# Optimization experiments

Hardware: AMD Instinct MI355X
Metric: run time of the kernel (lower is better)

## Reference

```python
import jax, jax.numpy as jnp
import numpy as np

EPS = 1e-07


def _softsplat(tenIn, tenFlow):
    # tenIn: [N, C, H, W], tenFlow: [N, 2, H, W]
    N, C, H, W = tenIn.shape
    dtype = tenIn.dtype
    gridX = jnp.arange(W, dtype=dtype)[None, None, :]  # [1,1,W]
    gridY = jnp.arange(H, dtype=dtype)[None, :, None]  # [1,H,1]
    fltX = gridX + tenFlow[:, 0]  # [N,H,W]
    fltY = gridY + tenFlow[:, 1]  # [N,H,W]
    finite = jnp.isfinite(fltX) & jnp.isfinite(fltY)
    fltX = jnp.where(finite, fltX, 0.0)
    fltY = jnp.where(finite, fltY, 0.0)
    nwX = jnp.floor(fltX)
    nwY = jnp.floor(fltY)
    b = jnp.arange(N, dtype=jnp.int32)[:, None, None]  # [N,1,1]
    tenIn_flat = jnp.transpose(tenIn, (0, 2, 3, 1)).reshape(-1, C)  # [N*H*W, C]
    out = jnp.zeros((N * H * W, C), dtype=dtype)
    # four bilinear corners: NW, NE, SW, SE
    for dx, dy in ((0, 0), (1, 0), (0, 1), (1, 1)):
        ix = nwX + dx
        iy = nwY + dy
        # bilinear weight, e.g. NW: (nwX+1-fltX)*(nwY+1-fltY)
        w = (1.0 - jnp.abs(fltX - ix)) * (1.0 - jnp.abs(fltY - iy))
        valid = finite & (ix >= 0) & (ix < W) & (iy >= 0) & (iy < H)
        w = jnp.where(valid, w, 0.0)  # zero-weight replaces torch's masked select
        ixi = jnp.clip(ix.astype(jnp.int32), 0, W - 1)
        iyi = jnp.clip(iy.astype(jnp.int32), 0, H - 1)
        idx = (b * (H * W) + iyi * W + ixi).reshape(-1)  # [N*H*W]
        out = out.at[idx].add(tenIn_flat * w.reshape(-1, 1))
    return jnp.transpose(out.reshape(N, H, W, C), (0, 3, 1, 2))


def setup_inputs() -> dict:
    key = jax.random.key(0)
    k1, k2, k3 = jax.random.split(key, 3)
    N, C, H, W = 4, 3, 1080, 1920
    tenIn = jax.random.normal(k1, (N, C, H, W), dtype=jnp.float32)
    tenFlow = jax.random.normal(k2, (N, 2, H, W), dtype=jnp.float32)
    tenMetric = jax.random.normal(k3, (N, 1, H, W), dtype=jnp.float32)
    return {"tenIn": tenIn, "tenFlow": tenFlow, "tenMetric": tenMetric}


def reference(tenIn, tenFlow, tenMetric):
    # mode='soft': concat [tenIn * exp(metric), exp(metric)], splat, normalize
    m = jnp.exp(tenMetric)
    tenCat = jnp.concatenate([tenIn * m, m], axis=1)  # [N, C+1, H, W]
    tenOut = _softsplat(tenCat, tenFlow)
    # mode_sub is None -> addeps normalization
    return tenOut[:, :-1] / (tenOut[:, -1:] + EPS)
```

## Files before the change

kernel.cpp:

```cpp
#include <hip/hip_runtime.h>
#include <math.h>

#define EPS 1e-7f

constexpr int Nn = 4, Hh = 1080, Ww = 1920;
constexpr int HW = Hh * Ww;
constexpr int TOTAL = Nn * HW;

constexpr int TW = 32, TH = 32;
constexpr int TXN = 60, TYN = 34;
constexpr int REACH = 5;
constexpr float NEAR_MAX = 5.0f;
constexpr int WINW = TW + 2 * REACH;
constexpr int WINH = TH + 2 * REACH;
constexpr int WINSZ = WINW * WINH;
constexpr int NCW = TW + 1;
constexpr int NCH = TH + 1;
constexpr int NCELLS = NCW * NCH;
constexpr int CNT_PAD = 1280;
constexpr int PADL = 8;
constexpr int NCHUNK = 12;
constexpr int TOTCH = NCHUNK * WINH;


__global__ __launch_bounds__(256) void far_scatter(
    const float* __restrict__ tenIn, const float* __restrict__ tenFlow,
    const float* __restrict__ tenMetric,
    unsigned int* __restrict__ farCount, float* __restrict__ farList,
    unsigned int farCap)
{
    int q = blockIdx.x * 256 + threadIdx.x;
    if (q >= TOTAL / 4) return;
    int n  = q / (HW / 4);
    int p  = (q - n * (HW / 4)) * 4;

    const float* __restrict__ f0 = tenFlow + (size_t)(n * 2 + 0) * HW;
    const float* __restrict__ f1 = f0 + HW;
    float4 fx4 = *(const float4*)(f0 + p);
    float4 fy4 = *(const float4*)(f1 + p);

    float mx = fmaxf(fmaxf(fabsf(fx4.x), fabsf(fx4.y)), fmaxf(fabsf(fx4.z), fabsf(fx4.w)));
    float my = fmaxf(fmaxf(fabsf(fy4.x), fabsf(fy4.y)), fmaxf(fabsf(fy4.z), fabsf(fy4.w)));
    if (!(mx > NEAR_MAX || my > NEAR_MAX)) return;

    int y = p / Ww;
    int xbase = p - y * Ww;
    float fxa[4] = {fx4.x, fx4.y, fx4.z, fx4.w};
    float fya[4] = {fy4.x, fy4.y, fy4.z, fy4.w};

#pragma unroll
    for (int k = 0; k < 4; ++k) {
        float fxv = fxa[k], fyv = fya[k];
        if (!(fabsf(fxv) > NEAR_MAX || fabsf(fyv) > NEAR_MAX)) continue;
        float fx = (float)(xbase + k) + fxv;
        float fy = (float)y + fyv;
        if (!isfinite(fx) || !isfinite(fy)) continue;
        if (!(fx > -1.0f && fx < (float)Ww && fy > -1.0f && fy < (float)Hh)) continue;

        int pp = p + k;
        float m  = expf(tenMetric[(size_t)n * HW + pp]);
        float v0 = tenIn[((size_t)n * 3 + 0) * HW + pp] * m;
        float v1 = tenIn[((size_t)n * 3 + 1) * HW + pp] * m;
        float v2 = tenIn[((size_t)n * 3 + 2) * HW + pp] * m;

        unsigned int slot = atomicAdd(farCount, 1u);
        if (slot < farCap) {
            float* ep = farList + (size_t)slot * 8;
            ep[0] = __int_as_float(n);
            ep[1] = fx; ep[2] = fy;
            ep[3] = v0; ep[4] = v1; ep[5] = v2; ep[6] = m;
            ep[7] = 0.0f;
        }
    }
}


__global__ __launch_bounds__(256, 3) void gather_splat(
    const float* __restrict__ tenIn, const float* __restrict__ tenFlow,
    const float* __restrict__ tenMetric,
    const float* __restrict__ farList, const unsigned int* __restrict__ farCount,
    unsigned int farCap, float* __restrict__ out)
{
    __shared__ float2 sFrac[WINSZ];
    __shared__ float4 sVal[WINSZ];
    __shared__ unsigned int sOff[CNT_PAD];
    __shared__ unsigned int sWsum[8];

    const int tx = blockIdx.x, ty = blockIdx.y, n = blockIdx.z;
    const int tX = tx * TW, tY = ty * TH;
    const int tid = threadIdx.x;

    for (int j = tid; j < CNT_PAD; j += 256) sOff[j] = 0u;
    __syncthreads();

    const float* __restrict__ f0 = tenFlow   + (size_t)(n * 2 + 0) * HW;
    const float* __restrict__ f1 = tenFlow   + (size_t)(n * 2 + 1) * HW;
    const float* __restrict__ mp = tenMetric + (size_t)n * HW;
    const float* __restrict__ i0 = tenIn + (size_t)(n * 3 + 0) * HW;
    const float* __restrict__ i1 = tenIn + (size_t)(n * 3 + 1) * HW;
    const float* __restrict__ i2 = tenIn + (size_t)(n * 3 + 2) * HW;

    unsigned int pk[2][4];
    float sfx[2][4], swy[2][4];

#pragma unroll
    for (int cc = 0; cc < 2; ++cc) {
#pragma unroll
        for (int k = 0; k < 4; ++k) { pk[cc][k] = 0xFFFFFFFFu; sfx[cc][k] = 0.f; swy[cc][k] = 0.f; }
        int cidx = tid + cc * 256;
        if (cidx >= TOTCH) continue;
        int wy = cidx / NCHUNK;
        int cx = cidx - wy * NCHUNK;
        int sy = tY - REACH + wy;
        int gx = tX - PADL + cx * 4;
        if (sy < 0 || sy >= Hh || gx < 0 || gx > Ww - 4) continue;
        int p = sy * Ww + gx;
        float4 fx4 = *(const float4*)(f0 + p);
        float4 fy4 = *(const float4*)(f1 + p);
        float fxa[4] = {fx4.x, fx4.y, fx4.z, fx4.w};
        float fya[4] = {fy4.x, fy4.y, fy4.z, fy4.w};
#pragma unroll
        for (int k = 0; k < 4; ++k) {
            int x = gx + k;
            if (x < tX - REACH || x >= tX + TW + REACH) continue;
            float fxv = fxa[k], fyv = fya[k];
            if (!(fabsf(fxv) <= NEAR_MAX && fabsf(fyv) <= NEAR_MAX)) continue;
            float fx = (float)x + fxv;
            float fy = (float)sy + fyv;
            float flx = floorf(fx), fly = floorf(fy);
            int lx0 = (int)flx - tX;
            int ly0 = (int)fly - tY;
            if (lx0 < -1 || lx0 >= TW || ly0 < -1 || ly0 >= TH) continue;
            int ci = (ly0 + 1) * NCW + (lx0 + 1);
            unsigned int sic = atomicAdd(&sOff[ci], 1u);
            pk[cc][k] = (sic << 16) | (unsigned int)ci;
            sfx[cc][k] = fx;
            swy[cc][k] = fy - fly;
        }
    }
    __syncthreads();

    unsigned int c0v, c1v, c2v, c3v, c4v;
    {
        int base = tid * 5;
        c0v = sOff[base];     c1v = sOff[base + 1]; c2v = sOff[base + 2];
        c3v = sOff[base + 3]; c4v = sOff[base + 4];
    }
    unsigned int tsum = c0v + c1v + c2v + c3v + c4v;
    unsigned int incl = tsum;
#pragma unroll
    for (int d = 1; d < 64; d <<= 1) {
        unsigned int v = __shfl_up(incl, d);
        if ((tid & 63) >= d) incl += v;
    }
    const int wv = tid >> 6;
    if ((tid & 63) == 63) sWsum[wv] = incl;
    __syncthreads();
    unsigned int woff = 0;
    {
        unsigned int w0 = sWsum[0], w1 = sWsum[1], w2 = sWsum[2];
        if (wv > 0) woff += w0;
        if (wv > 1) woff += w1;
        if (wv > 2) woff += w2;
    }
    unsigned int texcl = woff + incl - tsum;
    {
        int base = tid * 5;
        unsigned int o0 = texcl, o1 = o0 + c0v, o2 = o1 + c1v, o3 = o2 + c2v, o4 = o3 + c3v;
        sOff[base] = o0; sOff[base + 1] = o1; sOff[base + 2] = o2;
        sOff[base + 3] = o3; sOff[base + 4] = o4;
    }
    __syncthreads();

#pragma unroll
    for (int cc = 0; cc < 2; ++cc) {
        int cidx = tid + cc * 256;
        if (cidx >= TOTCH) continue;
        unsigned int allv = pk[cc][0] & pk[cc][1] & pk[cc][2] & pk[cc][3];
        if (allv == 0xFFFFFFFFu) continue;
        int wy = cidx / NCHUNK;
        int cx = cidx - wy * NCHUNK;
        int sy = tY - REACH + wy;
        int gx = tX - PADL + cx * 4;
        int p = sy * Ww + gx;
        float4 m4  = *(const float4*)(mp + p);
        float4 a04 = *(const float4*)(i0 + p);
        float4 a14 = *(const float4*)(i1 + p);
        float4 a24 = *(const float4*)(i2 + p);
        float ma[4]  = {m4.x,  m4.y,  m4.z,  m4.w};
        float a0a[4] = {a04.x, a04.y, a04.z, a04.w};
        float a1a[4] = {a14.x, a14.y, a14.z, a14.w};
        float a2a[4] = {a24.x, a24.y, a24.z, a24.w};
#pragma unroll
        for (int k = 0; k < 4; ++k) {
            unsigned int p_ = pk[cc][k];
            if (p_ == 0xFFFFFFFFu) continue;
            unsigned int ci  = p_ & 0xFFFFu;
            unsigned int sic = p_ >> 16;
            unsigned int slot = sOff[ci] + sic;
            float m = expf(ma[k]);
            sFrac[slot] = make_float2(sfx[cc][k], swy[cc][k]);
            sVal[slot]  = make_float4(a0a[k] * m, a1a[k] * m, a2a[k] * m, m);
        }
    }
    __syncthreads();

    const int r   = tid >> 3;
    const int g   = tid & 7;
    const int cc0 = g * 4;
    const float cx0f = (float)(tX + cc0);

    float4 acc0 = make_float4(0.f, 0.f, 0.f, 0.f);
    float4 acc1 = make_float4(0.f, 0.f, 0.f, 0.f);
    float4 acc2 = make_float4(0.f, 0.f, 0.f, 0.f);
    float4 acc3 = make_float4(0.f, 0.f, 0.f, 0.f);

    const unsigned int a0 = sOff[r * NCW + cc0];
    const unsigned int a1 = sOff[r * NCW + cc0 + 5];
    const unsigned int b0 = sOff[(r + 1) * NCW + cc0];
    const unsigned int b1 = sOff[(r + 1) * NCW + cc0 + 5];

#define SPLAT_BODY(AY_EXPR)                                               \
    do {                                                                  \
        float2 fr = sFrac[s];                                             \
        float4 v  = sVal[s];                                              \
        float ay  = (AY_EXPR);                                            \
        float dxf = fr.x - cx0f;                                          \
        float ax0 = fmaxf(0.f, 1.f - fabsf(dxf));                         \
        float ax1 = fmaxf(0.f, 1.f - fabsf(dxf - 1.f));                   \
        float ax2 = fmaxf(0.f, 1.f - fabsf(dxf - 2.f));                   \
        float ax3 = fmaxf(0.f, 1.f - fabsf(dxf - 3.f));                   \
        float w0 = ay * ax0, w1 = ay * ax1, w2 = ay * ax2, w3 = ay * ax3; \
        acc0.x += v.x * w0; acc0.y += v.y * w0; acc0.z += v.z * w0; acc0.w += v.w * w0; \
        acc1.x += v.x * w1; acc1.y += v.y * w1; acc1.z += v.z * w1; acc1.w += v.w * w1; \
        acc2.x += v.x * w2; acc2.y += v.y * w2; acc2.z += v.z * w2; acc2.w += v.w * w2; \
        acc3.x += v.x * w3; acc3.y += v.y * w3; acc3.z += v.z * w3; acc3.w += v.w * w3; \
    } while (0)

    for (unsigned int s = a0; s < a1; ++s) SPLAT_BODY(fr.y);
    for (unsigned int s = b0; s < b1; ++s) SPLAT_BODY(1.f - fr.y);
#undef SPLAT_BODY

    const int gy = tY + r;
    if (gy >= Hh) return;
    const int gx = tX + cc0;

    unsigned int fc = *farCount;
    if (fc > farCap) fc = farCap;
    const float gyf = (float)gy;
    const float gxf = (float)gx;
    for (unsigned int e = 0; e < fc; ++e) {
        const float* ep = farList + (size_t)e * 8;
        if (__float_as_int(ep[0]) != n) continue;
        float ffx = ep[1], ffy = ep[2];
        float ay = fmaxf(0.f, 1.f - fabsf(ffy - gyf));
        if (ay > 0.f) {
            float fv0 = ep[3], fv1 = ep[4], fv2 = ep[5], fm = ep[6];
            float d = ffx - gxf;
            float ax0 = fmaxf(0.f, 1.f - fabsf(d));
            float ax1 = fmaxf(0.f, 1.f - fabsf(d - 1.f));
            float ax2 = fmaxf(0.f, 1.f - fabsf(d - 2.f));
            float ax3 = fmaxf(0.f, 1.f - fabsf(d - 3.f));
            float w0 = ay * ax0, w1 = ay * ax1, w2 = ay * ax2, w3 = ay * ax3;
            acc0.x += fv0 * w0; acc0.y += fv1 * w0; acc0.z += fv2 * w0; acc0.w += fm * w0;
            acc1.x += fv0 * w1; acc1.y += fv1 * w1; acc1.z += fv2 * w1; acc1.w += fm * w1;
            acc2.x += fv0 * w2; acc2.y += fv1 * w2; acc2.z += fv2 * w2; acc2.w += fm * w2;
            acc3.x += fv0 * w3; acc3.y += fv1 * w3; acc3.z += fv2 * w3; acc3.w += fm * w3;
        }
    }

    const float inv0 = 1.0f / (acc0.w + EPS);
    const float inv1 = 1.0f / (acc1.w + EPS);
    const float inv2 = 1.0f / (acc2.w + EPS);
    const float inv3 = 1.0f / (acc3.w + EPS);

    const size_t pix = (size_t)gy * Ww + gx;
    float4 o;
    o = make_float4(acc0.x * inv0, acc1.x * inv1, acc2.x * inv2, acc3.x * inv3);
    *(float4*)(out + ((size_t)n * 3 + 0) * HW + pix) = o;
    o = make_float4(acc0.y * inv0, acc1.y * inv1, acc2.y * inv2, acc3.y * inv3);
    *(float4*)(out + ((size_t)n * 3 + 1) * HW + pix) = o;
    o = make_float4(acc0.z * inv0, acc1.z * inv1, acc2.z * inv2, acc3.z * inv3);
    *(float4*)(out + ((size_t)n * 3 + 2) * HW + pix) = o;
}

extern "C" void kernel_launch(void* const* d_in, const int* in_sizes, int n_in,
                              void* d_out, int out_size, void* d_ws, size_t ws_size,
                              hipStream_t stream) {
    const float* tenIn     = (const float*)d_in[0];
    const float* tenFlow   = (const float*)d_in[1];
    const float* tenMetric = (const float*)d_in[2];
    float* out = (float*)d_out;

    unsigned int* farCount = (unsigned int*)d_ws;
    float* farList = (float*)((char*)d_ws + 64);
    unsigned int farCap = (ws_size > 64) ? (unsigned int)((ws_size - 64) / 32) : 0;

    hipMemsetAsync(d_ws, 0, 64, stream);

    far_scatter<<<(TOTAL / 4 + 255) / 256, 256, 0, stream>>>(
        tenIn, tenFlow, tenMetric, farCount, farList, farCap);

    dim3 grid(TXN, TYN, Nn);
    gather_splat<<<grid, 256, 0, stream>>>(
        tenIn, tenFlow, tenMetric, farList, farCount, farCap, out);
}
```

Baseline: 307.5 us.

## Pack fractional offsets into 16-bit fixed point and split splat loop per cell

Measured after the change: 291.3 us. 5.3% less time.

```diff
diff --git a/kernel.cpp b/kernel.cpp
--- a/kernel.cpp
+++ b/kernel.cpp
@@ -17,10 +17,11 @@
 constexpr int NCW = TW + 1;
 constexpr int NCH = TH + 1;
 constexpr int NCELLS = NCW * NCH;
-constexpr int CNT_PAD = 1280;
+constexpr int NOFF = NCELLS + 1;
 constexpr int PADL = 8;
 constexpr int NCHUNK = 12;
 constexpr int TOTCH = NCHUNK * WINH;
+constexpr float INV64K = 1.52587890625e-5f;
 
 
 __global__ __launch_bounds__(256) void far_scatter(
@@ -75,22 +76,22 @@
 }
 
 
-__global__ __launch_bounds__(256, 3) void gather_splat(
+__global__ __launch_bounds__(256, 4) void gather_splat(
     const float* __restrict__ tenIn, const float* __restrict__ tenFlow,
     const float* __restrict__ tenMetric,
     const float* __restrict__ farList, const unsigned int* __restrict__ farCount,
     unsigned int farCap, float* __restrict__ out)
 {
-    __shared__ float2 sFrac[WINSZ];
     __shared__ float4 sVal[WINSZ];
-    __shared__ unsigned int sOff[CNT_PAD];
+    __shared__ unsigned int sPack[WINSZ];
+    __shared__ unsigned int sOff[NOFF];
     __shared__ unsigned int sWsum[8];
 
     const int tx = blockIdx.x, ty = blockIdx.y, n = blockIdx.z;
     const int tX = tx * TW, tY = ty * TH;
     const int tid = threadIdx.x;
 
-    for (int j = tid; j < CNT_PAD; j += 256) sOff[j] = 0u;
+    for (int j = tid; j < NOFF; j += 256) sOff[j] = 0u;
     __syncthreads();
 
     const float* __restrict__ f0 = tenFlow   + (size_t)(n * 2 + 0) * HW;
@@ -101,12 +102,12 @@
     const float* __restrict__ i2 = tenIn + (size_t)(n * 3 + 2) * HW;
 
     unsigned int pk[2][4];
-    float sfx[2][4], swy[2][4];
+    unsigned int spw[2][4];
 
 #pragma unroll
     for (int cc = 0; cc < 2; ++cc) {
 #pragma unroll
-        for (int k = 0; k < 4; ++k) { pk[cc][k] = 0xFFFFFFFFu; sfx[cc][k] = 0.f; swy[cc][k] = 0.f; }
+        for (int k = 0; k < 4; ++k) { pk[cc][k] = 0xFFFFFFFFu; spw[cc][k] = 0u; }
         int cidx = tid + cc * 256;
         if (cidx >= TOTCH) continue;
         int wy = cidx / NCHUNK;
@@ -134,14 +135,14 @@
             int ci = (ly0 + 1) * NCW + (lx0 + 1);
             unsigned int sic = atomicAdd(&sOff[ci], 1u);
             pk[cc][k] = (sic << 16) | (unsigned int)ci;
-            sfx[cc][k] = fx;
-            swy[cc][k] = fy - fly;
+            spw[cc][k] = __float2uint_rz((fx - flx) * 65536.0f)
+                       | (__float2uint_rz((fy - fly) * 65536.0f) << 16);
         }
     }
     __syncthreads();
 
-    unsigned int c0v, c1v, c2v, c3v, c4v;
-    {
+    unsigned int c0v = 0, c1v = 0, c2v = 0, c3v = 0, c4v = 0;
+    if (tid < 218) {
         int base = tid * 5;
         c0v = sOff[base];     c1v = sOff[base + 1]; c2v = sOff[base + 2];
         c3v = sOff[base + 3]; c4v = sOff[base + 4];
@@ -164,7 +165,7 @@
         if (wv > 2) woff += w2;
     }
     unsigned int texcl = woff + incl - tsum;
-    {
+    if (tid < 218) {
         int base = tid * 5;
         unsigned int o0 = texcl, o1 = o0 + c0v, o2 = o1 + c1v, o3 = o2 + c2v, o4 = o3 + c3v;
         sOff[base] = o0; sOff[base + 1] = o1; sOff[base + 2] = o2;
@@ -199,7 +200,7 @@
             unsigned int sic = p_ >> 16;
             unsigned int slot = sOff[ci] + sic;
             float m = expf(ma[k]);
-            sFrac[slot] = make_float2(sfx[cc][k], swy[cc][k]);
+            sPack[slot] = spw[cc][k];
             sVal[slot]  = make_float4(a0a[k] * m, a1a[k] * m, a2a[k] * m, m);
         }
     }
@@ -208,38 +209,50 @@
     const int r   = tid >> 3;
     const int g   = tid & 7;
     const int cc0 = g * 4;
-    const float cx0f = (float)(tX + cc0);
 
     float4 acc0 = make_float4(0.f, 0.f, 0.f, 0.f);
     float4 acc1 = make_float4(0.f, 0.f, 0.f, 0.f);
     float4 acc2 = make_float4(0.f, 0.f, 0.f, 0.f);
     float4 acc3 = make_float4(0.f, 0.f, 0.f, 0.f);
 
-    const unsigned int a0 = sOff[r * NCW + cc0];
-    const unsigned int a1 = sOff[r * NCW + cc0 + 5];
-    const unsigned int b0 = sOff[(r + 1) * NCW + cc0];
-    const unsigned int b1 = sOff[(r + 1) * NCW + cc0 + 5];
-
-#define SPLAT_BODY(AY_EXPR)                                               \
-    do {                                                                  \
-        float2 fr = sFrac[s];                                             \
-        float4 v  = sVal[s];                                              \
-        float ay  = (AY_EXPR);                                            \
-        float dxf = fr.x - cx0f;                                          \
-        float ax0 = fmaxf(0.f, 1.f - fabsf(dxf));                         \
-        float ax1 = fmaxf(0.f, 1.f - fabsf(dxf - 1.f));                   \
-        float ax2 = fmaxf(0.f, 1.f - fabsf(dxf - 2.f));                   \
-        float ax3 = fmaxf(0.f, 1.f - fabsf(dxf - 3.f));                   \
-        float w0 = ay * ax0, w1 = ay * ax1, w2 = ay * ax2, w3 = ay * ax3; \
-        acc0.x += v.x * w0; acc0.y += v.y * w0; acc0.z += v.z * w0; acc0.w += v.w * w0; \
-        acc1.x += v.x * w1; acc1.y += v.y * w1; acc1.z += v.z * w1; acc1.w += v.w * w1; \
-        acc2.x += v.x * w2; acc2.y += v.y * w2; acc2.z += v.z * w2; acc2.w += v.w * w2; \
-        acc3.x += v.x * w3; acc3.y += v.y * w3; acc3.z += v.z * w3; acc3.w += v.w * w3; \
-    } while (0)
-
-    for (unsigned int s = a0; s < a1; ++s) SPLAT_BODY(fr.y);
-    for (unsigned int s = b0; s < b1; ++s) SPLAT_BODY(1.f - fr.y);
-#undef SPLAT_BODY
+#define SUBR(S0, S1, ROWA, HASL, HASR, ACCL, ACCR)                        \
+    for (unsigned int s = (S0); s < (S1); ++s) {                          \
+        unsigned int pw = sPack[s];                                       \
+        float4 v = sVal[s];                                               \
+        float fracx = (float)(pw & 0xFFFFu) * INV64K;                     \
+        float wy1q  = (float)(pw >> 16)     * INV64K;                     \
+        float ay = (ROWA) ? wy1q : (1.0f - wy1q);                         \
+        float wr = ay * fracx;                                            \
+        float wl = ay - wr;                                               \
+        if (HASL) { ACCL.x += v.x*wl; ACCL.y += v.y*wl;                   \
+                    ACCL.z += v.z*wl; ACCL.w += v.w*wl; }                 \
+        if (HASR) { ACCR.x += v.x*wr; ACCR.y += v.y*wr;                   \
+                    ACCR.z += v.z*wr; ACCR.w += v.w*wr; }                 \
+    }
+
+    {
+        const int baseA = r * NCW + cc0;
+        unsigned int o0 = sOff[baseA],     o1 = sOff[baseA + 1];
+        unsigned int o2 = sOff[baseA + 2], o3 = sOff[baseA + 3];
+        unsigned int o4 = sOff[baseA + 4], o5 = sOff[baseA + 5];
+        SUBR(o0, o1, true, false, true,  acc0, acc0)
+        SUBR(o1, o2, true, true,  true,  acc0, acc1)
+        SUBR(o2, o3, true, true,  true,  acc1, acc2)
+        SUBR(o3, o4, true, true,  true,  acc2, acc3)
+        SUBR(o4, o5, true, true,  false, acc3, acc0)
+    }
+    {
+        const int baseB = (r + 1) * NCW + cc0;
+        unsigned int o0 = sOff[baseB],     o1 = sOff[baseB + 1];
+        unsigned int o2 = sOff[baseB + 2], o3 = sOff[baseB + 3];
+        unsigned int o4 = sOff[baseB + 4], o5 = sOff[baseB + 5];
+        SUBR(o0, o1, false, false, true,  acc0, acc0)
+        SUBR(o1, o2, false, true,  true,  acc0, acc1)
+        SUBR(o2, o3, false, true,  true,  acc1, acc2)
+        SUBR(o3, o4, false, true,  true,  acc2, acc3)
+        SUBR(o4, o5, false, true,  false, acc3, acc0)
+    }
+#undef SUBR
 
     const int gy = tY + r;
     if (gy >= Hh) return;
```
